# Performance work log

Hardware: AMD Instinct MI355X
Metric: run time of the kernel (lower is better)

Reference implementation:

```python
import jax, jax.numpy as jnp
import numpy as np
import math

T, N, F, A, NH = 2048, 64, 64, 64, 8
QG, QH, DG, DH = 256, 256, 256, 256
HORIZON = 16


def setup_inputs() -> dict:
    key = jax.random.key(0)
    ks = jax.random.split(key, 12)
    s = 0.05  # xavier-ish scale
    return {
        "x_fix": jax.random.normal(ks[0], (T, F), jnp.float32),
        "x_att": jax.random.normal(ks[1], (T, N, A), jnp.float32),
        "train_horizon": HORIZON,
        # query GRUCell: input = fix + 2*A*NH
        "q_gru_w_ih": jax.random.normal(ks[2], (3 * QG, F + 2 * A * NH), jnp.float32) * s,
        "q_gru_w_hh": jax.random.normal(ks[3], (3 * QG, QG), jnp.float32) * s,
        "q_gru_b_ih": jnp.zeros((3 * QG,), jnp.float32),
        "q_gru_b_hh": jnp.zeros((3 * QG,), jnp.float32),
        # q_hidden: input = QG + F + A*NH
        "q_hid_w": jax.random.normal(ks[4], (QH, QG + F + A * NH), jnp.float32) * s,
        "q_hid_b": jnp.zeros((QH,), jnp.float32),
        "weight_q": jax.random.normal(ks[5], (QH, A * NH), jnp.float32) * s,
        # decoder GRU: input = F + A*NH
        "dec_gru_w_ih": jax.random.normal(ks[6], (3 * DG, F + A * NH), jnp.float32) * s,
        "dec_gru_w_hh": jax.random.normal(ks[7], (3 * DG, DG), jnp.float32) * s,
        "dec_gru_b_ih": jnp.zeros((3 * DG,), jnp.float32),
        "dec_gru_b_hh": jnp.zeros((3 * DG,), jnp.float32),
        # dec_hidden: input = DG + F + A*NH + A
        "dec_hid_w": jax.random.normal(ks[8], (DH, DG + F + A * NH + A), jnp.float32) * s,
        "dec_hid_b": jnp.zeros((DH,), jnp.float32),
        "dec_out_w": jax.random.normal(ks[9], (A, DH), jnp.float32) * s,
        "dec_out_b": jnp.zeros((A,), jnp.float32),
    }


def _gru_cell(x, h, w_ih, w_hh, b_ih, b_hh):
    """PyTorch GRUCell math (gate order r,z,n)."""
    gi = w_ih @ x + b_ih
    gh = w_hh @ h + b_hh
    ir, iz, in_ = jnp.split(gi, 3)
    hr, hz, hn = jnp.split(gh, 3)
    r = jax.nn.sigmoid(ir + hr)
    z = jax.nn.sigmoid(iz + hz)
    n = jnp.tanh(in_ + r * hn)
    return (1.0 - z) * n + z * h


def reference(x_fix, x_att, train_horizon,
              q_gru_w_ih, q_gru_w_hh, q_gru_b_ih, q_gru_b_hh,
              q_hid_w, q_hid_b, weight_q,
              dec_gru_w_ih, dec_gru_w_hh, dec_gru_b_ih, dec_gru_b_hh,
              dec_hid_w, dec_hid_b, dec_out_w, dec_out_b):
    t, n_obj, a = x_att.shape
    nh_a = weight_q.shape[1]
    nh = nh_a // a
    scale = 1.0 / math.sqrt(a)

    # ---- recurrent query generation (sequential over time) ----
    def step(carry, inp):
        h, query = carry
        fix_t, att_t = inp                                   # [F], [N, A]
        attw = jax.nn.softmax((query.reshape(nh, a) @ att_t.T) * scale, axis=1)  # [NH, N]
        att_v = (attw @ att_t).reshape(-1)                   # [NH*A]
        h2 = _gru_cell(jnp.concatenate([fix_t, att_v, query]), h,
                       q_gru_w_ih, q_gru_w_hh, q_gru_b_ih, q_gru_b_hh)
        hid = jax.nn.relu(q_hid_w @ jnp.concatenate([h2, fix_t, att_v]) + q_hid_b)
        query2 = hid @ weight_q
        return (h2, query2), (attw, att_v)

    h0 = jnp.zeros((q_gru_w_hh.shape[1],), x_fix.dtype)
    q0 = jnp.ones((nh_a,), x_fix.dtype)
    (q_gru_n, query_n), (attw, att_a) = jax.lax.scan(step, (h0, q0), (x_fix, x_att))

    # ---- decoder (training path; dropout_p=0, noise_std=0 -> identity) ----
    hz = train_horizon
    # replicate-pad attw back hz steps in time, drop last hz: dec_attw[t] = attw[max(t-hz,0)]
    dec_attw = jnp.concatenate(
        [jnp.broadcast_to(attw[:1], (hz,) + attw.shape[1:]), attw[:-hz]], axis=0)  # [T, NH, N]
    dec_att_a = jnp.einsum('thn,tnd->thd', dec_attw, x_att).reshape(t, -1)          # [T, NH*A]
    dec_x = jnp.concatenate([x_fix, dec_att_a], axis=-1)                            # [T, F+NH*A]

    def dec_step(hd, xt):
        hd2 = _gru_cell(xt, hd, dec_gru_w_ih, dec_gru_w_hh, dec_gru_b_ih, dec_gru_b_hh)
        return hd2, hd2

    dg0 = jnp.zeros((dec_gru_w_hh.shape[1],), x_fix.dtype)
    dec_gru_n, dec_gru_a = jax.lax.scan(dec_step, dg0, dec_x)                       # [T, DG]

    feat = jnp.concatenate([dec_gru_a, dec_x], axis=-1)                             # [T, DG+F+NH*A]
    feat_b = jnp.broadcast_to(feat[:, None, :], (t, n_obj, feat.shape[-1]))
    inp = jnp.concatenate([feat_b, x_att], axis=-1)                                 # [T, N, DG+F+NH*A+A]
    hid = jax.nn.relu(inp @ dec_hid_w.T + dec_hid_b)
    pred = jax.nn.relu(hid @ dec_out_w.T + dec_out_b)                               # [T, N, A]

    return pred, attw, q_gru_n, dec_gru_n, query_n
```

## Files before the change

### kernel.cpp

```cpp
#include <hip/hip_runtime.h>
#include <math.h>

#define TT 2048
#define HZ 16
#define NBLK 32
#define NTH 512

#define OUT_ATTW   (2048*64*64)
#define OUT_QGRU   (OUT_ATTW + 2048*8*64)
#define OUT_DECGRU (OUT_QGRU + 256)
#define OUT_QN     (OUT_DECGRU + 256)

#define WSO_MB1    0
#define WSO_QACC   8192
#define WSO_QCNT   14336
#define WSO_ZEND   14464
#define WSO_GIFIX  14464
#define WSO_HIDFIX (WSO_GIFIX + 2048*768*4)
#define WSO_W2T    (WSO_HIDFIX + 2048*256*4)
#define WSO_DAVA   (WSO_W2T + 256*64*4)
#define WSO_DECH   (WSO_DAVA + 2048*512*4)
#define WSO_FEAT   (WSO_DECH + 2048*256*4)
#define WSO_SBUF   (WSO_FEAT + 2048*832*4)

__device__ __forceinline__ float warp_sum(float v) {
#pragma unroll
  for (int o = 32; o > 0; o >>= 1) v += __shfl_down(v, o, 64);
  return v;
}
__device__ __forceinline__ float warp_max(float v) {
#pragma unroll
  for (int o = 32; o > 0; o >>= 1) v = fmaxf(v, __shfl_down(v, o, 64));
  return v;
}
__device__ __forceinline__ float sigf(float x) { return 1.f / (1.f + __expf(-x)); }
__device__ __forceinline__ float dot4(float4 a, float4 b) {
  return a.x*b.x + a.y*b.y + a.z*b.z + a.w*b.w;
}
__device__ __forceinline__ unsigned long long aload64(const unsigned long long* p) {
  return __hip_atomic_load(p, __ATOMIC_RELAXED, __HIP_MEMORY_SCOPE_AGENT);
}
__device__ __forceinline__ void astore64(unsigned long long* p, unsigned long long v) {
  __hip_atomic_store(p, v, __ATOMIC_RELAXED, __HIP_MEMORY_SCOPE_AGENT);
}
__device__ __forceinline__ unsigned long long mbpack(float f, unsigned tag) {
  return ((unsigned long long)tag << 32) | (unsigned long long)__float_as_uint(f);
}
__device__ __forceinline__ float mbpoll(const unsigned long long* p, unsigned tag) {
  unsigned long long v = aload64(p);
  while ((unsigned)(v >> 32) != tag) {
    __builtin_amdgcn_s_sleep(1);
    v = aload64(p);
  }
  return __uint_as_float((unsigned)v);
}

__global__ void transpose_k(const float* __restrict__ w2,
                            float* __restrict__ w2T) {
  int e = blockIdx.x * 256 + threadIdx.x;
  int r = e >> 6, a = e & 63;
  w2T[e] = w2[a * 256 + r];
}

__global__ void __launch_bounds__(256) gemm64(
    const float* __restrict__ X, int ldx,
    const float* __restrict__ W, int ldw, int woff,
    const float* __restrict__ bias,
    float* __restrict__ C, int crows, int K) {
  __shared__ float Xs[64 * 65];
  __shared__ float Ws[64 * 65];
  int t0 = blockIdx.x * 64, r0 = blockIdx.y * 64;
  int tid = threadIdx.x;
  int u = tid & 15, v = tid >> 4;
  float acc[4][4];
#pragma unroll
  for (int i = 0; i < 4; i++)
#pragma unroll
    for (int j = 0; j < 4; j++) acc[i][j] = 0.f;

  for (int kc = 0; kc < K; kc += 64) {
    for (int idx = tid; idx < 4096; idx += 256) {
      int row = idx >> 6, col = idx & 63;
      Xs[row * 65 + col] = X[(size_t)(t0 + row) * ldx + kc + col];
      Ws[row * 65 + col] = W[(size_t)(r0 + row) * ldw + woff + kc + col];
    }
    __syncthreads();
#pragma unroll 8
    for (int k = 0; k < 64; k++) {
      float xs[4], ws[4];
#pragma unroll
      for (int i = 0; i < 4; i++) xs[i] = Xs[(v + 16 * i) * 65 + k];
#pragma unroll
      for (int j = 0; j < 4; j++) ws[j] = Ws[(u + 16 * j) * 65 + k];
#pragma unroll
      for (int i = 0; i < 4; i++)
#pragma unroll
        for (int j = 0; j < 4; j++) acc[i][j] += xs[i] * ws[j];
    }
    __syncthreads();
  }
#pragma unroll
  for (int i = 0; i < 4; i++)
#pragma unroll
    for (int j = 0; j < 4; j++) {
      int t = t0 + v + 16 * i, r = r0 + u + 16 * j;
      C[(size_t)t * crows + r] = acc[i][j] + bias[r];
    }
}

__global__ void __launch_bounds__(512) seq_kernel(
    const float* __restrict__ x_fix,
    const float* __restrict__ x_att,
    const float* __restrict__ w_ih,
    const float* __restrict__ w_hh,
    const float* __restrict__ b_hh,
    const float* __restrict__ q_hid_w,
    const float* __restrict__ wq,
    const float* __restrict__ dwih,
    const float* __restrict__ dwhh,
    const float* __restrict__ dbih,
    const float* __restrict__ dbhh,
    const float* __restrict__ gi_fix,
    const float* __restrict__ hid_fix,
    unsigned long long* __restrict__ mb1,
    float* __restrict__ qacc,
    unsigned* __restrict__ qcnt,
    float* __restrict__ dava,
    float* __restrict__ dec_hist,
    float* __restrict__ out) {
  __shared__ float att_s[64 * 65];
  __shared__ float ring_s[16][512];
  __shared__ __align__(16) float avq_s[1024];
  __shared__ float qk_s[512];
  __shared__ __align__(16) float xcat_s[576];
  __shared__ __align__(16) float hid8_s[8];
  __shared__ __align__(16) float h_s[256];
  __shared__ __align__(16) float dech_s[256];
  __shared__ float g_s[4][8];
  __shared__ float dg_s[4][8];

  const int tid = threadIdx.x;
  const int bid = blockIdx.x;
  const int lane = tid & 63, wv = tid >> 6;

  int rowsQ[3];
#pragma unroll
  for (int k = 0; k < 3; k++) {
    int m = wv * 3 + k;
    rowsQ[k] = ((m >> 3) * 256) + bid * 8 + (m & 7);
  }

  float4 wGi[3][4];
  float4 wGh[3];
  float bhh_r[3], dbi_r[3], dbh_r[3];
#pragma unroll
  for (int k = 0; k < 3; k++) {
    const float4* Wi = (const float4*)(w_ih + (size_t)rowsQ[k] * 1088 + 64);
#pragma unroll
    for (int c0 = 0; c0 < 4; c0++) wGi[k][c0] = Wi[lane + 64 * c0];
    wGh[k] = ((const float4*)(w_hh + (size_t)rowsQ[k] * 256))[lane];
    bhh_r[k] = b_hh[rowsQ[k]];
    dbi_r[k] = dbih[rowsQ[k]];
    dbh_r[k] = dbhh[rowsQ[k]];
  }
  float4 wBq[3];
  {
    const float4* W = (const float4*)(q_hid_w + (size_t)(bid * 8 + wv) * 832);
    wBq[0] = W[lane];
    wBq[1] = W[80 + lane];
    wBq[2] = W[144 + lane];
  }
  float wqr[8];
#pragma unroll
  for (int r = 0; r < 8; r++) wqr[r] = wq[(size_t)(bid * 8 + r) * 512 + tid];

  auto dec_gates = [&]() {
    float accg[3], acch[3];
#pragma unroll
    for (int k = 0; k < 3; k++) { accg[k] = 0.f; acch[k] = 0.f; }
    const float4* x4 = (const float4*)xcat_s;
#pragma unroll
    for (int c0 = 0; c0 < 3; c0++) {
      int c = lane + 64 * c0;
      if (c < 144) {
        float4 v = x4[c];
#pragma unroll
        for (int k = 0; k < 3; k++) {
          const float4* W = (const float4*)(dwih + (size_t)rowsQ[k] * 576);
          accg[k] += dot4(W[c], v);
        }
      }
    }
    {
      float4 vh = ((const float4*)dech_s)[lane];
#pragma unroll
      for (int k = 0; k < 3; k++) {
        const float4* Wh = (const float4*)(dwhh + (size_t)rowsQ[k] * 256);
        acch[k] += dot4(Wh[lane], vh);
      }
    }
#pragma unroll
    for (int k = 0; k < 3; k++) {
      int m = wv * 3 + k;
      int gate = m >> 3, idx = m & 7;
      if (gate < 2) {
        float s = warp_sum(accg[k] + acch[k]);
        if (lane == 0) dg_s[gate][idx] = s + dbi_r[k] + dbh_r[k];
      } else {
        float sg = warp_sum(accg[k]);
        float sh = warp_sum(acch[k]);
        if (lane == 0) { dg_s[2][idx] = sg + dbi_r[k]; dg_s[3][idx] = sh + dbh_r[k]; }
      }
    }
  };

  for (int i = tid; i < 1024; i += NTH) avq_s[i] = (i >= 512) ? 1.f : 0.f;
  if (tid < 256) { h_s[tid] = 0.f; dech_s[tid] = 0.f; }
  {
    const float4* g4 = (const float4*)x_att;
    float4 a = g4[tid * 2], b = g4[tid * 2 + 1];
    int row = tid >> 3, c0 = (tid & 7) * 8;
    float* d = &att_s[row * 65 + c0];
    d[0]=a.x; d[1]=a.y; d[2]=a.z; d[3]=a.w; d[4]=b.x; d[5]=b.y; d[6]=b.z; d[7]=b.w;
  }
  if (tid < 64) xcat_s[tid] = x_fix[tid];
  __syncthreads();

  for (int t = 0; t <= TT; ++t) {
    if (t > 0) {
      {
        float f = mbpoll(mb1 + (size_t)((t - 1) & 1) * 512 + tid, (unsigned)t);
        int b = tid >> 4, j = tid & 15;
        if (j < 8) h_s[b * 8 + j] = f;
        else dech_s[b * 8 + j - 8] = f;
        if (t >= 2 && tid < 16)
          __hip_atomic_store(&qacc[(size_t)((t - 1) % 3) * 512 + bid * 16 + tid],
                             0.f, __ATOMIC_RELAXED, __HIP_MEMORY_SCOPE_AGENT);
      }
      __syncthreads();
      {
        float hfx = hid_fix[(size_t)(t - 1) * 256 + bid * 8 + wv];
        const float4* h4 = (const float4*)h_s;
        const float4* a4 = (const float4*)avq_s;
        float acc = dot4(wBq[0], h4[lane]) + dot4(wBq[1], a4[lane]) +
                    dot4(wBq[2], a4[64 + lane]);
        float s = warp_sum(acc);
        if (lane == 0) hid8_s[wv] = fmaxf(s + hfx, 0.f);
      }
      __syncthreads();
      {
        float hv[8];
#pragma unroll
        for (int r = 0; r < 8; r++) hv[r] = hid8_s[r];
        float partial = 0.f;
#pragma unroll
        for (int r = 0; r < 8; r++) partial += hv[r] * wqr[r];
        __hip_atomic_fetch_add(&qacc[(size_t)(t % 3) * 512 + tid], partial,
                               __ATOMIC_RELAXED, __HIP_MEMORY_SCOPE_AGENT);
      }
      if (t < TT) {
        {
          const float* rg = ring_s[(t >= 16) ? (t & 15) : 0];
          float dv = 0.f;
#pragma unroll 8
          for (int n = 0; n < 64; n++) dv += rg[wv * 64 + n] * att_s[n * 65 + lane];
          xcat_s[64 + wv * 64 + lane] = dv;
        }
        __syncthreads();
        dec_gates();
        asm volatile("s_waitcnt vmcnt(0)" ::: "memory");
        __syncthreads();
        if (tid == 0)
          __hip_atomic_fetch_add(qcnt, 1u, __ATOMIC_RELAXED,
                                 __HIP_MEMORY_SCOPE_AGENT);
        if (tid < 8) {
          float r = sigf(dg_s[0][tid]), z = sigf(dg_s[1][tid]);
          float nn = tanhf(dg_s[2][tid] + r * dg_s[3][tid]);
          float d2 = (1.f - z) * nn + z * dech_s[bid * 8 + tid];
          astore64(&mb1[(size_t)(t & 1) * 512 + bid * 16 + 8 + tid],
                   mbpack(d2, (unsigned)(t + 1)));
          dec_hist[(size_t)t * 256 + bid * 8 + tid] = d2;
        } else if (tid >= 16 && tid < 32) {
          int k2 = tid - 16;
          dava[(size_t)t * 512 + bid * 16 + k2] = xcat_s[64 + bid * 16 + k2];
        }
      } else {
        asm volatile("s_waitcnt vmcnt(0)" ::: "memory");
        __syncthreads();
        if (tid == 0)
          __hip_atomic_fetch_add(qcnt, 1u, __ATOMIC_RELAXED,
                                 __HIP_MEMORY_SCOPE_AGENT);
      }
      {
        unsigned target = 32u * (unsigned)t;
        while (__hip_atomic_load(qcnt, __ATOMIC_RELAXED,
                                 __HIP_MEMORY_SCOPE_AGENT) < target)
          __builtin_amdgcn_s_sleep(1);
        float qv = __hip_atomic_load(&qacc[(size_t)(t % 3) * 512 + tid],
                                     __ATOMIC_RELAXED, __HIP_MEMORY_SCOPE_AGENT);
        avq_s[512 + tid] = qv;
        if (t == TT) {
          if (bid == 0) {
            if (tid < 256) {
              out[OUT_QGRU + tid] = h_s[tid];
              out[OUT_DECGRU + tid] = dech_s[tid];
            }
            out[OUT_QN + tid] = qv;
          }
          break;
        }
      }
      __syncthreads();
    }

    float4 pfa, pfb;
    {
      int tn = (t + 1 < TT) ? t + 1 : t;
      const float4* g4 = (const float4*)(x_att + (size_t)tn * 4096);
      pfa = g4[tid * 2];
      pfb = g4[tid * 2 + 1];
    }
    float gfx[3];
#pragma unroll
    for (int k = 0; k < 3; k++) gfx[k] = gi_fix[(size_t)t * 768 + rowsQ[k]];
    {
      float acc = 0.f;
#pragma unroll 16
      for (int a = 0; a < 64; a++)
        acc += avq_s[512 + wv * 64 + a] * att_s[lane * 65 + a];
      acc *= 0.125f;
      float m = __shfl(warp_max(acc), 0, 64);
      float e = __expf(acc - m);
      float s = __shfl(warp_sum(e), 0, 64);
      qk_s[wv * 64 + lane] = e / s;
    }
    {
      float av = 0.f;
#pragma unroll 8
      for (int n = 0; n < 64; n++)
        av += qk_s[wv * 64 + n] * att_s[n * 65 + lane];
      avq_s[wv * 64 + lane] = av;
    }
    if (t == 0) {
      float dv = 0.f;
#pragma unroll 8
      for (int n = 0; n < 64; n++)
        dv += qk_s[wv * 64 + n] * att_s[n * 65 + lane];
      xcat_s[64 + wv * 64 + lane] = dv;
    }
    __syncthreads();
    {
      float accg[3], acch[3];
#pragma unroll
      for (int k = 0; k < 3; k++) { accg[k] = 0.f; acch[k] = 0.f; }
      const float4* in4 = (const float4*)avq_s;
#pragma unroll
      for (int c0 = 0; c0 < 4; c0++) {
        float4 v = in4[lane + 64 * c0];
#pragma unroll
        for (int k = 0; k < 3; k++) accg[k] += dot4(wGi[k][c0], v);
      }
      {
        float4 vh = ((const float4*)h_s)[lane];
#pragma unroll
        for (int k = 0; k < 3; k++) acch[k] += dot4(wGh[k], vh);
      }
#pragma unroll
      for (int k = 0; k < 3; k++) {
        int m = wv * 3 + k;
        int gate = m >> 3, idx = m & 7;
        if (gate < 2) {
          float s = warp_sum(accg[k] + acch[k]);
          if (lane == 0) g_s[gate][idx] = s + gfx[k] + bhh_r[k];
        } else {
          float sg = warp_sum(accg[k]);
          float sh = warp_sum(acch[k]);
          if (lane == 0) { g_s[2][idx] = sg + gfx[k]; g_s[3][idx] = sh + bhh_r[k]; }
        }
      }
    }
    if (t == 0) dec_gates();
    __syncthreads();
    if (tid < 8) {
      float r = sigf(g_s[0][tid]), z = sigf(g_s[1][tid]);
      float nn = tanhf(g_s[2][tid] + r * g_s[3][tid]);
      float h2 = (1.f - z) * nn + z * h_s[bid * 8 + tid];
      astore64(&mb1[(size_t)(t & 1) * 512 + bid * 16 + tid],
               mbpack(h2, (unsigned)(t + 1)));
    } else if (t == 0 && tid < 16) {
      int i = tid - 8;
      float r = sigf(dg_s[0][i]), z = sigf(dg_s[1][i]);
      float nn = tanhf(dg_s[2][i] + r * dg_s[3][i]);
      float d2 = (1.f - z) * nn + z * dech_s[bid * 8 + i];
      astore64(&mb1[(size_t)(t & 1) * 512 + bid * 16 + tid],
               mbpack(d2, (unsigned)(t + 1)));
      dec_hist[(size_t)t * 256 + bid * 8 + i] = d2;
    }
    if (tid < 16) {
      out[OUT_ATTW + (size_t)t * 512 + bid * 16 + tid] = qk_s[bid * 16 + tid];
      if (t == 0)
        dava[(size_t)t * 512 + bid * 16 + tid] = xcat_s[64 + bid * 16 + tid];
    }
    ring_s[t & 15][tid] = qk_s[tid];
    {
      int row = tid >> 3, c0 = (tid & 7) * 8;
      float* d = &att_s[row * 65 + c0];
      d[0]=pfa.x; d[1]=pfa.y; d[2]=pfa.z; d[3]=pfa.w;
      d[4]=pfb.x; d[5]=pfb.y; d[6]=pfb.z; d[7]=pfb.w;
    }
    if (tid >= 448) {
      int i = tid - 448;
      int tn = (t + 1 < TT) ? t + 1 : t;
      xcat_s[i] = x_fix[tn * 64 + i];
    }
  }
}

__global__ void featcopy(const float* __restrict__ dec_hist,
                         const float* __restrict__ x_fix,
                         const float* __restrict__ dava,
                         float* __restrict__ feat) {
  int t = blockIdx.x, tid = threadIdx.x;
  float* f = feat + (size_t)t * 832;
  f[tid] = dec_hist[(size_t)t * 256 + tid];
  if (tid < 64) f[256 + tid] = x_fix[t * 64 + tid];
  for (int i = tid; i < 512; i += 256) f[320 + i] = dava[(size_t)t * 512 + i];
}

__global__ void __launch_bounds__(256) final_k(
    const float* __restrict__ x_att,
    const float* __restrict__ s,
    const float* __restrict__ w1,
    const float* __restrict__ w2T,
    const float* __restrict__ b2,
    float* __restrict__ pred) {
  __shared__ float att_s[4096];
  __shared__ float s_s[256];
  __shared__ float hid_s[32 * 256];
  int t = blockIdx.x, tid = threadIdx.x, lane = tid & 63, wv = tid >> 6;
  for (int i = tid; i < 4096; i += 256) att_s[i] = x_att[(size_t)t * 4096 + i];
  s_s[tid] = s[(size_t)t * 256 + tid];
  float4 w1v[16];
  const float4* W1a4 = (const float4*)(w1 + (size_t)tid * 896 + 832);
#pragma unroll
  for (int q = 0; q < 16; q++) w1v[q] = W1a4[q];
  float bb = b2[lane];
  __syncthreads();
  for (int ch = 0; ch < 2; ch++) {
    for (int nl = 0; nl < 32; nl++) {
      int n = ch * 32 + nl;
      const float4* a4 = (const float4*)(att_s + n * 64);
      float acc = s_s[tid];
#pragma unroll
      for (int q = 0; q < 16; q++) acc += dot4(w1v[q], a4[q]);
      hid_s[nl * 256 + tid] = fmaxf(acc, 0.f);
    }
    __syncthreads();
    float accb[8];
#pragma unroll
    for (int j = 0; j < 8; j++) accb[j] = bb;
    for (int r = 0; r < 256; r++) {
      float w = w2T[r * 64 + lane];
#pragma unroll
      for (int j = 0; j < 8; j++) accb[j] += w * hid_s[(wv * 8 + j) * 256 + r];
    }
#pragma unroll
    for (int j = 0; j < 8; j++) {
      int n = ch * 32 + wv * 8 + j;
      pred[(size_t)t * 4096 + n * 64 + lane] = fmaxf(accb[j], 0.f);
    }
    __syncthreads();
  }
}

extern "C" void kernel_launch(void* const* d_in, const int* in_sizes, int n_in,
                              void* d_out, int out_size, void* d_ws, size_t ws_size,
                              hipStream_t stream) {
  const float* x_fix = (const float*)d_in[0];
  const float* x_att = (const float*)d_in[1];
  const float* qwih = (const float*)d_in[3];
  const float* qwhh = (const float*)d_in[4];
  const float* qbih = (const float*)d_in[5];
  const float* qbhh = (const float*)d_in[6];
  const float* qhw = (const float*)d_in[7];
  const float* qhb = (const float*)d_in[8];
  const float* wq = (const float*)d_in[9];
  const float* dwih = (const float*)d_in[10];
  const float* dwhh = (const float*)d_in[11];
  const float* dbih = (const float*)d_in[12];
  const float* dbhh = (const float*)d_in[13];
  const float* w1 = (const float*)d_in[14];
  const float* b1 = (const float*)d_in[15];
  const float* w2 = (const float*)d_in[16];
  const float* b2 = (const float*)d_in[17];
  float* out = (float*)d_out;

  char* ws = (char*)d_ws;
  unsigned long long* mb1 = (unsigned long long*)(ws + WSO_MB1);
  float* qacc = (float*)(ws + WSO_QACC);
  unsigned* qcnt = (unsigned*)(ws + WSO_QCNT);
  float* gi_fix = (float*)(ws + WSO_GIFIX);
  float* hid_fix = (float*)(ws + WSO_HIDFIX);
  float* w2T = (float*)(ws + WSO_W2T);
  float* dava = (float*)(ws + WSO_DAVA);
  float* dec_hist = (float*)(ws + WSO_DECH);
  float* feat = (float*)(ws + WSO_FEAT);
  float* sbuf = (float*)(ws + WSO_SBUF);

  hipMemsetAsync(ws, 0, WSO_ZEND, stream);

  transpose_k<<<64, 256, 0, stream>>>(w2, w2T);
  gemm64<<<dim3(32, 12), 256, 0, stream>>>(x_fix, 64, qwih, 1088, 0, qbih,
                                           gi_fix, 768, 64);
  gemm64<<<dim3(32, 4), 256, 0, stream>>>(x_fix, 64, qhw, 832, 256, qhb,
                                          hid_fix, 256, 64);

  seq_kernel<<<NBLK, NTH, 0, stream>>>(x_fix, x_att, qwih, qwhh, qbhh,
                                       qhw, wq, dwih, dwhh, dbih, dbhh,
                                       gi_fix, hid_fix, mb1, qacc, qcnt,
                                       dava, dec_hist, out);

  featcopy<<<2048, 256, 0, stream>>>(dec_hist, x_fix, dava, feat);
  gemm64<<<dim3(32, 4), 256, 0, stream>>>(feat, 832, w1, 896, 0, b1,
                                          sbuf, 256, 832);
  final_k<<<2048, 256, 0, stream>>>(x_att, sbuf, w1, w2T, b2, out);
}
```

Before: 18.38 ms.

## Hoist decoder input-gate GEMV ahead of mailbox poll to overlap with latency

Moves the attention-weighted feature computation and the decoder GRU input-side dot products (W_ih·x) ahead of the inter-block mailbox poll. Only the recurrent W_hh·h part remains after the poll. This overlaps independent work with the cross-block synchronization wait on the serial critical path. It adds an extra __syncthreads at the end of each iteration and keeps three partial-sum accumulators live across the poll, which raises register pressure.

```diff
diff --git a/kernel.cpp b/kernel.cpp
--- a/kernel.cpp
+++ b/kernel.cpp
@@ -227,7 +227,34 @@
   __syncthreads();
 
   for (int t = 0; t <= TT; ++t) {
+    float accg_d[3] = {0.f, 0.f, 0.f};
     if (t > 0) {
+      if (t < TT) {
+        {
+          const float* rg = ring_s[(t >= 16) ? (t & 15) : 0];
+          float dv = 0.f;
+#pragma unroll 8
+          for (int n = 0; n < 64; n++)
+            dv += rg[wv * 64 + n] * att_s[n * 65 + lane];
+          xcat_s[64 + wv * 64 + lane] = dv;
+        }
+        __syncthreads();
+        {
+          const float4* x4 = (const float4*)xcat_s;
+#pragma unroll
+          for (int c0 = 0; c0 < 3; c0++) {
+            int c = lane + 64 * c0;
+            if (c < 144) {
+              float4 v = x4[c];
+#pragma unroll
+              for (int k = 0; k < 3; k++) {
+                const float4* W = (const float4*)(dwih + (size_t)rowsQ[k] * 576);
+                accg_d[k] += dot4(W[c], v);
+              }
+            }
+          }
+        }
+      }
       {
         float f = mbpoll(mb1 + (size_t)((t - 1) & 1) * 512 + tid, (unsigned)t);
         int b = tid >> 4, j = tid & 15;
@@ -260,14 +287,31 @@
       }
       if (t < TT) {
         {
-          const float* rg = ring_s[(t >= 16) ? (t & 15) : 0];
-          float dv = 0.f;
-#pragma unroll 8
-          for (int n = 0; n < 64; n++) dv += rg[wv * 64 + n] * att_s[n * 65 + lane];
-          xcat_s[64 + wv * 64 + lane] = dv;
-        }
-        __syncthreads();
-        dec_gates();
+          float acch[3];
+#pragma unroll
+          for (int k = 0; k < 3; k++) acch[k] = 0.f;
+          {
+            float4 vh = ((const float4*)dech_s)[lane];
+#pragma unroll
+            for (int k = 0; k < 3; k++) {
+              const float4* Wh = (const float4*)(dwhh + (size_t)rowsQ[k] * 256);
+              acch[k] += dot4(Wh[lane], vh);
+            }
+          }
+#pragma unroll
+          for (int k = 0; k < 3; k++) {
+            int m = wv * 3 + k;
+            int gate = m >> 3, idx = m & 7;
+            if (gate < 2) {
+              float s = warp_sum(accg_d[k] + acch[k]);
+              if (lane == 0) dg_s[gate][idx] = s + dbi_r[k] + dbh_r[k];
+            } else {
+              float sg = warp_sum(accg_d[k]);
+              float sh = warp_sum(acch[k]);
+              if (lane == 0) { dg_s[2][idx] = sg + dbi_r[k]; dg_s[3][idx] = sh + dbh_r[k]; }
+            }
+          }
+        }
         asm volatile("s_waitcnt vmcnt(0)" ::: "memory");
         __syncthreads();
         if (tid == 0)
@@ -413,6 +457,7 @@
       int tn = (t + 1 < TT) ? t + 1 : t;
       xcat_s[i] = x_fix[tn * 64 + i];
     }
+    __syncthreads();
   }
 }
 
```

Measured after the change: 18.72 ms. About the same (+1.8%).

## Compute query hidden/projection redundantly per block instead of atomic cross-block reduction

Applied to the files above, without the earlier changes.

Every block now computes the full 256-wide query-hidden layer and the 512-wide query projection itself, reading a transposed q_hid weight and wq from global/L2. This removes the atomic accumulation buffer, the global counter, and the spin-wait barrier across all 32 blocks each step. The decoder GRU step is also moved to run after the query GRU gate publish in every step. The cost is many more redundant global weight reads per step (about 1.5K rows by 256 columns per block), which may be L2-bandwidth limited.

```diff
diff --git a/kernel.cpp b/kernel.cpp
--- a/kernel.cpp
+++ b/kernel.cpp
@@ -2,7 +2,6 @@
 #include <math.h>
 
 #define TT 2048
-#define HZ 16
 #define NBLK 32
 #define NTH 512
 
@@ -12,9 +11,7 @@
 #define OUT_QN     (OUT_DECGRU + 256)
 
 #define WSO_MB1    0
-#define WSO_QACC   8192
-#define WSO_QCNT   14336
-#define WSO_ZEND   14464
+#define WSO_ZEND   8192
 #define WSO_GIFIX  14464
 #define WSO_HIDFIX (WSO_GIFIX + 2048*768*4)
 #define WSO_W2T    (WSO_HIDFIX + 2048*256*4)
@@ -22,6 +19,7 @@
 #define WSO_DECH   (WSO_DAVA + 2048*512*4)
 #define WSO_FEAT   (WSO_DECH + 2048*256*4)
 #define WSO_SBUF   (WSO_FEAT + 2048*832*4)
+#define WSO_QHWT   WSO_FEAT
 
 __device__ __forceinline__ float warp_sum(float v) {
 #pragma unroll
@@ -60,6 +58,13 @@
   int e = blockIdx.x * 256 + threadIdx.x;
   int r = e >> 6, a = e & 63;
   w2T[e] = w2[a * 256 + r];
+}
+
+__global__ void transpose_qhw(const float* __restrict__ qhw,
+                              float* __restrict__ qhwT) {
+  int c = blockIdx.x, r = threadIdx.x;
+  int col = (c < 256) ? c : (c + 64);
+  qhwT[(size_t)c * 256 + r] = qhw[(size_t)r * 832 + col];
 }
 
 __global__ void __launch_bounds__(256) gemm64(
@@ -114,7 +119,7 @@
     const float* __restrict__ w_ih,
     const float* __restrict__ w_hh,
     const float* __restrict__ b_hh,
-    const float* __restrict__ q_hid_w,
+    const float* __restrict__ qhwT,
     const float* __restrict__ wq,
     const float* __restrict__ dwih,
     const float* __restrict__ dwhh,
@@ -123,8 +128,6 @@
     const float* __restrict__ gi_fix,
     const float* __restrict__ hid_fix,
     unsigned long long* __restrict__ mb1,
-    float* __restrict__ qacc,
-    unsigned* __restrict__ qcnt,
     float* __restrict__ dava,
     float* __restrict__ dec_hist,
     float* __restrict__ out) {
@@ -133,7 +136,7 @@
   __shared__ __align__(16) float avq_s[1024];
   __shared__ float qk_s[512];
   __shared__ __align__(16) float xcat_s[576];
-  __shared__ __align__(16) float hid8_s[8];
+  __shared__ __align__(16) float hid_sh[256];
   __shared__ __align__(16) float h_s[256];
   __shared__ __align__(16) float dech_s[256];
   __shared__ float g_s[4][8];
@@ -142,6 +145,7 @@
   const int tid = threadIdx.x;
   const int bid = blockIdx.x;
   const int lane = tid & 63, wv = tid >> 6;
+  float* hpart_s = qk_s;
 
   int rowsQ[3];
 #pragma unroll
@@ -163,16 +167,6 @@
     dbi_r[k] = dbih[rowsQ[k]];
     dbh_r[k] = dbhh[rowsQ[k]];
   }
-  float4 wBq[3];
-  {
-    const float4* W = (const float4*)(q_hid_w + (size_t)(bid * 8 + wv) * 832);
-    wBq[0] = W[lane];
-    wBq[1] = W[80 + lane];
-    wBq[2] = W[144 + lane];
-  }
-  float wqr[8];
-#pragma unroll
-  for (int r = 0; r < 8; r++) wqr[r] = wq[(size_t)(bid * 8 + r) * 512 + tid];
 
   auto dec_gates = [&]() {
     float accg[3], acch[3];
@@ -233,82 +227,46 @@
         int b = tid >> 4, j = tid & 15;
         if (j < 8) h_s[b * 8 + j] = f;
         else dech_s[b * 8 + j - 8] = f;
-        if (t >= 2 && tid < 16)
-          __hip_atomic_store(&qacc[(size_t)((t - 1) % 3) * 512 + bid * 16 + tid],
-                             0.f, __ATOMIC_RELAXED, __HIP_MEMORY_SCOPE_AGENT);
       }
       __syncthreads();
       {
-        float hfx = hid_fix[(size_t)(t - 1) * 256 + bid * 8 + wv];
-        const float4* h4 = (const float4*)h_s;
-        const float4* a4 = (const float4*)avq_s;
-        float acc = dot4(wBq[0], h4[lane]) + dot4(wBq[1], a4[lane]) +
-                    dot4(wBq[2], a4[64 + lane]);
-        float s = warp_sum(acc);
-        if (lane == 0) hid8_s[wv] = fmaxf(s + hfx, 0.f);
+        int r = tid & 255;
+        float acc = 0.f;
+        if (tid < 256) {
+#pragma unroll 8
+          for (int c = 0; c < 256; c++)
+            acc += h_s[c] * qhwT[(size_t)c * 256 + r];
+#pragma unroll 8
+          for (int c = 0; c < 128; c++)
+            acc += avq_s[c] * qhwT[(size_t)(256 + c) * 256 + r];
+        } else {
+#pragma unroll 8
+          for (int c = 128; c < 512; c++)
+            acc += avq_s[c] * qhwT[(size_t)(256 + c) * 256 + r];
+        }
+        hpart_s[tid] = acc;
       }
       __syncthreads();
+      if (tid < 256)
+        hid_sh[tid] = fmaxf(hpart_s[tid] + hpart_s[256 + tid] +
+                            hid_fix[(size_t)(t - 1) * 256 + tid], 0.f);
+      __syncthreads();
+      float q = 0.f;
       {
-        float hv[8];
-#pragma unroll
-        for (int r = 0; r < 8; r++) hv[r] = hid8_s[r];
-        float partial = 0.f;
-#pragma unroll
-        for (int r = 0; r < 8; r++) partial += hv[r] * wqr[r];
-        __hip_atomic_fetch_add(&qacc[(size_t)(t % 3) * 512 + tid], partial,
-                               __ATOMIC_RELAXED, __HIP_MEMORY_SCOPE_AGENT);
-      }
-      if (t < TT) {
-        {
-          const float* rg = ring_s[(t >= 16) ? (t & 15) : 0];
-          float dv = 0.f;
-#pragma unroll 8
-          for (int n = 0; n < 64; n++) dv += rg[wv * 64 + n] * att_s[n * 65 + lane];
-          xcat_s[64 + wv * 64 + lane] = dv;
+        const float* wqp = wq + tid;
+#pragma unroll 8
+        for (int r = 0; r < 256; r++) q += hid_sh[r] * wqp[(size_t)r * 512];
+      }
+      avq_s[512 + tid] = q;
+      if (t == TT) {
+        if (bid == 0) {
+          if (tid < 256) {
+            out[OUT_QGRU + tid] = h_s[tid];
+            out[OUT_DECGRU + tid] = dech_s[tid];
+          }
+          out[OUT_QN + tid] = q;
         }
-        __syncthreads();
-        dec_gates();
-        asm volatile("s_waitcnt vmcnt(0)" ::: "memory");
-        __syncthreads();
-        if (tid == 0)
-          __hip_atomic_fetch_add(qcnt, 1u, __ATOMIC_RELAXED,
-                                 __HIP_MEMORY_SCOPE_AGENT);
-        if (tid < 8) {
-          float r = sigf(dg_s[0][tid]), z = sigf(dg_s[1][tid]);
-          float nn = tanhf(dg_s[2][tid] + r * dg_s[3][tid]);
-          float d2 = (1.f - z) * nn + z * dech_s[bid * 8 + tid];
-          astore64(&mb1[(size_t)(t & 1) * 512 + bid * 16 + 8 + tid],
-                   mbpack(d2, (unsigned)(t + 1)));
-          dec_hist[(size_t)t * 256 + bid * 8 + tid] = d2;
-        } else if (tid >= 16 && tid < 32) {
-          int k2 = tid - 16;
-          dava[(size_t)t * 512 + bid * 16 + k2] = xcat_s[64 + bid * 16 + k2];
-        }
-      } else {
-        asm volatile("s_waitcnt vmcnt(0)" ::: "memory");
-        __syncthreads();
-        if (tid == 0)
-          __hip_atomic_fetch_add(qcnt, 1u, __ATOMIC_RELAXED,
-                                 __HIP_MEMORY_SCOPE_AGENT);
-      }
-      {
-        unsigned target = 32u * (unsigned)t;
-        while (__hip_atomic_load(qcnt, __ATOMIC_RELAXED,
-                                 __HIP_MEMORY_SCOPE_AGENT) < target)
-          __builtin_amdgcn_s_sleep(1);
-        float qv = __hip_atomic_load(&qacc[(size_t)(t % 3) * 512 + tid],
-                                     __ATOMIC_RELAXED, __HIP_MEMORY_SCOPE_AGENT);
-        avq_s[512 + tid] = qv;
-        if (t == TT) {
-          if (bid == 0) {
-            if (tid < 256) {
-              out[OUT_QGRU + tid] = h_s[tid];
-              out[OUT_DECGRU + tid] = dech_s[tid];
-            }
-            out[OUT_QN + tid] = qv;
-          }
-          break;
-        }
+        break;
       }
       __syncthreads();
     }
@@ -340,13 +298,6 @@
       for (int n = 0; n < 64; n++)
         av += qk_s[wv * 64 + n] * att_s[n * 65 + lane];
       avq_s[wv * 64 + lane] = av;
-    }
-    if (t == 0) {
-      float dv = 0.f;
-#pragma unroll 8
-      for (int n = 0; n < 64; n++)
-        dv += qk_s[wv * 64 + n] * att_s[n * 65 + lane];
-      xcat_s[64 + wv * 64 + lane] = dv;
     }
     __syncthreads();
     {
@@ -379,7 +330,6 @@
         }
       }
     }
-    if (t == 0) dec_gates();
     __syncthreads();
     if (tid < 8) {
       float r = sigf(g_s[0][tid]), z = sigf(g_s[1][tid]);
@@ -387,20 +337,30 @@
       float h2 = (1.f - z) * nn + z * h_s[bid * 8 + tid];
       astore64(&mb1[(size_t)(t & 1) * 512 + bid * 16 + tid],
                mbpack(h2, (unsigned)(t + 1)));
-    } else if (t == 0 && tid < 16) {
-      int i = tid - 8;
-      float r = sigf(dg_s[0][i]), z = sigf(dg_s[1][i]);
-      float nn = tanhf(dg_s[2][i] + r * dg_s[3][i]);
-      float d2 = (1.f - z) * nn + z * dech_s[bid * 8 + i];
-      astore64(&mb1[(size_t)(t & 1) * 512 + bid * 16 + tid],
+    }
+    {
+      const float* rg = (t == 0) ? &qk_s[0] : ring_s[(t >= 16) ? (t & 15) : 0];
+      float dv = 0.f;
+#pragma unroll 8
+      for (int n = 0; n < 64; n++) dv += rg[wv * 64 + n] * att_s[n * 65 + lane];
+      xcat_s[64 + wv * 64 + lane] = dv;
+    }
+    __syncthreads();
+    dec_gates();
+    __syncthreads();
+    if (tid < 8) {
+      float r = sigf(dg_s[0][tid]), z = sigf(dg_s[1][tid]);
+      float nn = tanhf(dg_s[2][tid] + r * dg_s[3][tid]);
+      float d2 = (1.f - z) * nn + z * dech_s[bid * 8 + tid];
+      astore64(&mb1[(size_t)(t & 1) * 512 + bid * 16 + 8 + tid],
                mbpack(d2, (unsigned)(t + 1)));
-      dec_hist[(size_t)t * 256 + bid * 8 + i] = d2;
-    }
-    if (tid < 16) {
+      dec_hist[(size_t)t * 256 + bid * 8 + tid] = d2;
+    } else if (tid >= 16 && tid < 32) {
+      int k2 = tid - 16;
+      dava[(size_t)t * 512 + bid * 16 + k2] = xcat_s[64 + bid * 16 + k2];
+    }
+    if (tid < 16)
       out[OUT_ATTW + (size_t)t * 512 + bid * 16 + tid] = qk_s[bid * 16 + tid];
-      if (t == 0)
-        dava[(size_t)t * 512 + bid * 16 + tid] = xcat_s[64 + bid * 16 + tid];
-    }
     ring_s[t & 15][tid] = qk_s[tid];
     {
       int row = tid >> 3, c0 = (tid & 7) * 8;
@@ -497,8 +457,6 @@
 
   char* ws = (char*)d_ws;
   unsigned long long* mb1 = (unsigned long long*)(ws + WSO_MB1);
-  float* qacc = (float*)(ws + WSO_QACC);
-  unsigned* qcnt = (unsigned*)(ws + WSO_QCNT);
   float* gi_fix = (float*)(ws + WSO_GIFIX);
   float* hid_fix = (float*)(ws + WSO_HIDFIX);
   float* w2T = (float*)(ws + WSO_W2T);
@@ -506,18 +464,20 @@
   float* dec_hist = (float*)(ws + WSO_DECH);
   float* feat = (float*)(ws + WSO_FEAT);
   float* sbuf = (float*)(ws + WSO_SBUF);
+  float* qhwT = (float*)(ws + WSO_QHWT);
 
   hipMemsetAsync(ws, 0, WSO_ZEND, stream);
 
   transpose_k<<<64, 256, 0, stream>>>(w2, w2T);
+  transpose_qhw<<<768, 256, 0, stream>>>(qhw, qhwT);
   gemm64<<<dim3(32, 12), 256, 0, stream>>>(x_fix, 64, qwih, 1088, 0, qbih,
                                            gi_fix, 768, 64);
   gemm64<<<dim3(32, 4), 256, 0, stream>>>(x_fix, 64, qhw, 832, 256, qhb,
                                           hid_fix, 256, 64);
 
   seq_kernel<<<NBLK, NTH, 0, stream>>>(x_fix, x_att, qwih, qwhh, qbhh,
-                                       qhw, wq, dwih, dwhh, dbih, dbhh,
-                                       gi_fix, hid_fix, mb1, qacc, qcnt,
+                                       qhwT, wq, dwih, dwhh, dbih, dbhh,
+                                       gi_fix, hid_fix, mb1,
                                        dava, dec_hist, out);
 
   featcopy<<<2048, 256, 0, stream>>>(dec_hist, x_fix, dava, feat);
```

After: 42.76 ms. 2.33x slower.
